# Optimization experiments

Measured on AMD Instinct MI355X. Metric: run time of the kernel, lower is better.

## Reference

```python
import jax, jax.numpy as jnp
import numpy as np

N_HEADS = 32
KV_HEADS = 8
HEAD_DIM = 128
N_REP = N_HEADS // KV_HEADS


def _rope(x, cos, sin):
    # x: [b, s, h, d]; cos/sin: [s, d//2]
    xr = x[..., 0::2]
    xi = x[..., 1::2]
    c = cos[None, :, None, :]
    s = sin[None, :, None, :]
    or_ = xr * c - xi * s
    oi_ = xr * s + xi * c
    return jnp.stack([or_, oi_], axis=-1).reshape(x.shape)


def setup_inputs() -> dict:
    key = jax.random.key(0)
    ks = jax.random.split(key, 9)
    b, s, dim = 32, 1, 4096
    scale = 1.0 / np.sqrt(dim)
    inp = {
        "x": jax.random.normal(ks[0], (b, s, dim), jnp.float32),
        "wq": jax.random.normal(ks[1], (4096, 4096), jnp.float32) * scale,
        "wk": jax.random.normal(ks[2], (1024, 4096), jnp.float32) * scale,
        "wv": jax.random.normal(ks[3], (1024, 4096), jnp.float32) * scale,
        "wo": jax.random.normal(ks[4], (4096, 4096), jnp.float32) * scale,
        "freqs_cos": jax.random.uniform(ks[5], (s, HEAD_DIM // 2), jnp.float32),
        "freqs_sin": jax.random.uniform(ks[6], (s, HEAD_DIM // 2), jnp.float32),
        "cache_k": jax.random.normal(ks[7], (32, 2048, KV_HEADS, HEAD_DIM), jnp.float32),
        "cache_v": jax.random.normal(ks[8], (32, 2048, KV_HEADS, HEAD_DIM), jnp.float32),
        "start_pos": 2047,
    }
    return inp


def reference(x, wq, wk, wv, wo, freqs_cos, freqs_sin, cache_k, cache_v, start_pos):
    b, s, dim = x.shape
    # projections (nn.Linear: y = x @ W^T)
    xq = (x @ wq.T).reshape(b, s, N_HEADS, HEAD_DIM)
    xk = (x @ wk.T).reshape(b, s, KV_HEADS, HEAD_DIM)
    xv = (x @ wv.T).reshape(b, s, KV_HEADS, HEAD_DIM)
    # inline RoPE on q and k
    xq = _rope(xq, freqs_cos, freqs_sin)
    xk = _rope(xk, freqs_cos, freqs_sin)
    # KV-cache write (start_pos is a static Python int)
    cache_k = cache_k.at[:b, start_pos:start_pos + s].set(xk)
    cache_v = cache_v.at[:b, start_pos:start_pos + s].set(xv)
    t = start_pos + s
    keys = cache_k[:b, :t]    # [b, t, kv, d]
    values = cache_v[:b, :t]  # [b, t, kv, d]
    # GQA: group queries per kv head instead of materializing repeat_kv copies
    q = xq.reshape(b, s, KV_HEADS, N_REP, HEAD_DIM)
    scores = jnp.einsum("bqhrd,bkhd->bhrqk", q, keys) / np.sqrt(HEAD_DIM)
    probs = jax.nn.softmax(scores.astype(jnp.float32), axis=-1).astype(xq.dtype)
    out = jnp.einsum("bhrqk,bkhd->bqhrd", probs, values)
    out = out.reshape(b, s, N_HEADS * HEAD_DIM)
    return out @ wo.T
```

## Files before the change

kernel.cpp:

```cpp
#include <hip/hip_runtime.h>
#include <hip/hip_bf16.h>
#include <math.h>

#define KSPLIT 16
#define KCHUNK 256
#define BJ 128

__global__ __launch_bounds__(256) void gemv_part_kernel(
    const float* __restrict__ x,
    const float* __restrict__ w0,
    const float* __restrict__ w1,
    const float* __restrict__ w2,
    int jb1, int jb2,
    int off0, int off1, int off2,
    int ncols,
    float* __restrict__ part)
{
  __shared__ float xt[KCHUNK][32];
  int jb = blockIdx.x, ks = blockIdx.y;
  int k0 = ks * KCHUNK;
  const float* w; int colOff, jbase;
  if (jb < jb1)      { w = w0; colOff = off0; jbase = jb * BJ; }
  else if (jb < jb2) { w = w1; colOff = off1; jbase = (jb - jb1) * BJ; }
  else               { w = w2; colOff = off2; jbase = (jb - jb2) * BJ; }
  int tid = threadIdx.x;
  {
    int b = tid & 31, kg = tid >> 5;
    const float* xr = x + (size_t)b * 4096 + k0 + kg * 32;
    #pragma unroll
    for (int i = 0; i < 8; i++) {
      float4 v = *(const float4*)(xr + i * 4);
      int k = kg * 32 + i * 4;
      xt[k + 0][b] = v.x; xt[k + 1][b] = v.y;
      xt[k + 2][b] = v.z; xt[k + 3][b] = v.w;
    }
  }
  __syncthreads();
  int bg = tid & 7, jg = tid >> 3;
  const float* wb = w + (size_t)(jbase + jg * 4) * 4096 + k0;
  float acc[4][4] = {};
  #pragma unroll 4
  for (int k4 = 0; k4 < KCHUNK / 4; k4++) {
    float wr[4][4], xv[4][4];
    #pragma unroll
    for (int jj = 0; jj < 4; jj++) {
      float4 t = *(const float4*)(wb + (size_t)jj * 4096 + k4 * 4);
      wr[jj][0] = t.x; wr[jj][1] = t.y; wr[jj][2] = t.z; wr[jj][3] = t.w;
    }
    #pragma unroll
    for (int c = 0; c < 4; c++) {
      float4 t = *(const float4*)(&xt[k4 * 4 + c][bg * 4]);
      xv[c][0] = t.x; xv[c][1] = t.y; xv[c][2] = t.z; xv[c][3] = t.w;
    }
    #pragma unroll
    for (int jj = 0; jj < 4; jj++)
      #pragma unroll
      for (int bb = 0; bb < 4; bb++)
        acc[jj][bb] += wr[jj][0] * xv[0][bb] + wr[jj][1] * xv[1][bb]
                     + wr[jj][2] * xv[2][bb] + wr[jj][3] * xv[3][bb];
  }
  #pragma unroll
  for (int jj = 0; jj < 4; jj++) {
    int col = colOff + jbase + jg * 4 + jj;
    #pragma unroll
    for (int bb = 0; bb < 4; bb++) {
      int b_ = bg * 4 + bb;
      part[((size_t)ks * 32 + b_) * ncols + col] = acc[jj][bb];
    }
  }
}

__global__ __launch_bounds__(256) void reduce_rope_kernel(
    const float* __restrict__ part, int ncols,
    const float* __restrict__ cosv, const float* __restrict__ sinv,
    int ropeEnd, float* __restrict__ outb)
{
  int idx = blockIdx.x * 256 + threadIdx.x;
  int np = ncols >> 1;
  int b = idx / np;
  int cp = idx - b * np;
  int col = cp * 2;
  float e = 0.f, o = 0.f;
  #pragma unroll
  for (int ks = 0; ks < KSPLIT; ks++) {
    float2 v = *(const float2*)(part + ((size_t)ks * 32 + b) * ncols + col);
    e += v.x; o += v.y;
  }
  if (col < ropeEnd) {
    int fi = (col & 127) >> 1;
    float c = cosv[fi], s = sinv[fi];
    float ne = e * c - o * s;
    float no = e * s + o * c;
    e = ne; o = no;
  }
  *(float2*)(outb + (size_t)b * ncols + col) = make_float2(e, o);
}

__global__ __launch_bounds__(256) void attn_kernel(
    const float* __restrict__ qkv,
    const float* __restrict__ cache_k,
    const float* __restrict__ cache_v,
    const int* __restrict__ spp,
    float* __restrict__ attn_part)
{
  __shared__ float q_s[4][128];
  __shared__ float kn_s[128], vn_s[128];
  __shared__ float p_s[4][4][64];
  __shared__ float comb_m[4][4], comb_l[4][4];
  __shared__ float comb_o[4][4][128];
  int bid = blockIdx.x;
  int ts = bid & 1, h = (bid >> 1) & 7, b = bid >> 4;
  int sp = *spp;
  const float scale = 0.088388347648318447f;
  int tid = threadIdx.x;
  {
    int i0 = tid * 2;
    int r = i0 >> 7, d = i0 & 127;
    q_s[r][d]     = qkv[(size_t)b * 6144 + (h * 4 + r) * 128 + d]     * scale;
    q_s[r][d + 1] = qkv[(size_t)b * 6144 + (h * 4 + r) * 128 + d + 1] * scale;
  }
  if (tid < 128) {
    kn_s[tid] = qkv[(size_t)b * 6144 + 4096 + h * 128 + tid];
    vn_s[tid] = qkv[(size_t)b * 6144 + 5120 + h * 128 + tid];
  }
  __syncthreads();
  int wave = tid >> 6, lane = tid & 63;
  int base0 = ts * 1024 + wave * 256;
  float m[4]    = {-INFINITY, -INFINITY, -INFINITY, -INFINITY};
  float lsum[4] = {0.f, 0.f, 0.f, 0.f};
  float o0[4] = {0.f, 0.f, 0.f, 0.f}, o1[4] = {0.f, 0.f, 0.f, 0.f};
  const float* Kb = cache_k + (size_t)b * 2048 * 1024 + h * 128;
  const float* Vb = cache_v + (size_t)b * 2048 * 1024 + h * 128;

  for (int c = 0; c < 4; c++) {
    int tbase = base0 + c * 64;
    int t = tbase + lane;
    float s[4];
    if (t < sp) {
      s[0] = s[1] = s[2] = s[3] = 0.f;
      const float* Kr = Kb + (size_t)t * 1024;
      #pragma unroll 8
      for (int d4 = 0; d4 < 32; d4++) {
        float4 kv = *(const float4*)(Kr + d4 * 4);
        #pragma unroll
        for (int r = 0; r < 4; r++) {
          float4 qv = *(const float4*)(&q_s[r][d4 * 4]);
          s[r] += kv.x * qv.x + kv.y * qv.y + kv.z * qv.z + kv.w * qv.w;
        }
      }
    } else {
      s[0] = s[1] = s[2] = s[3] = -INFINITY;
    }
    #pragma unroll
    for (int r = 0; r < 4; r++) {
      float cm = s[r];
      #pragma unroll
      for (int off = 32; off >= 1; off >>= 1) cm = fmaxf(cm, __shfl_xor(cm, off));
      float nm = fmaxf(m[r], cm);
      float alpha, p;
      if (nm == -INFINITY) { alpha = 1.f; p = 0.f; }
      else {
        alpha = __expf(m[r] - nm);
        p = (s[r] == -INFINITY) ? 0.f : __expf(s[r] - nm);
      }
      m[r] = nm;
      lsum[r] = lsum[r] * alpha + p;
      o0[r] *= alpha; o1[r] *= alpha;
      p_s[wave][r][lane] = p;
    }
    #pragma unroll 8
    for (int tt = 0; tt < 64; tt++) {
      const float* Vr = Vb + (size_t)(tbase + tt) * 1024;
      float2 vv = *(const float2*)(Vr + lane * 2);
      #pragma unroll
      for (int r = 0; r < 4; r++) {
        float p = p_s[wave][r][tt];
        o0[r] += p * vv.x; o1[r] += p * vv.y;
      }
    }
  }

  if (wave == 0 && sp >= ts * 1024 && sp < ts * 1024 + 1024) {
    float sNew[4];
    #pragma unroll
    for (int r = 0; r < 4; r++) {
      float a = q_s[r][lane * 2] * kn_s[lane * 2]
              + q_s[r][lane * 2 + 1] * kn_s[lane * 2 + 1];
      #pragma unroll
      for (int off = 32; off >= 1; off >>= 1) a += __shfl_xor(a, off);
      sNew[r] = a;
    }
    #pragma unroll
    for (int r = 0; r < 4; r++) {
      float nm = fmaxf(m[r], sNew[r]);
      float alpha = (m[r] == -INFINITY) ? 0.f : __expf(m[r] - nm);
      float p = __expf(sNew[r] - nm);
      m[r] = nm;
      lsum[r] = lsum[r] * alpha + ((lane == 0) ? p : 0.f);
      o0[r] = o0[r] * alpha + p * vn_s[lane * 2];
      o1[r] = o1[r] * alpha + p * vn_s[lane * 2 + 1];
    }
  }

  #pragma unroll
  for (int r = 0; r < 4; r++) {
    float L = lsum[r];
    #pragma unroll
    for (int off = 32; off >= 1; off >>= 1) L += __shfl_xor(L, off);
    if (lane == 0) { comb_m[wave][r] = m[r]; comb_l[wave][r] = L; }
    comb_o[wave][r][lane * 2]     = o0[r];
    comb_o[wave][r][lane * 2 + 1] = o1[r];
  }
  __syncthreads();
  {
    int r = tid >> 6, dp = tid & 63;
    float gm = fmaxf(fmaxf(comb_m[0][r], comb_m[1][r]),
                     fmaxf(comb_m[2][r], comb_m[3][r]));
    float L = 0.f, O0 = 0.f, O1 = 0.f;
    #pragma unroll
    for (int wv = 0; wv < 4; wv++) {
      float mm = comb_m[wv][r];
      float al = (mm == -INFINITY) ? 0.f : __expf(mm - gm);
      L  += comb_l[wv][r] * al;
      O0 += comb_o[wv][r][dp * 2]     * al;
      O1 += comb_o[wv][r][dp * 2 + 1] * al;
    }
    float* ap = attn_part + ((((size_t)ts * 32 + b) * 8 + h) * 4 + r) * 130;
    if (dp == 0) { ap[0] = gm; ap[1] = L; }
    ap[2 + dp * 2] = O0;
    ap[3 + dp * 2] = O1;
  }
}

__global__ __launch_bounds__(256) void attn_combine_kernel(
    const float* __restrict__ attn_part, float* __restrict__ attn)
{
  int idx = blockIdx.x * 256 + threadIdx.x;
  int d = idx & 127;
  int r = (idx >> 7) & 3;
  int h = (idx >> 9) & 7;
  int b = idx >> 12;
  const float* p0 = attn_part + (((size_t)(0 * 32 + b) * 8 + h) * 4 + r) * 130;
  const float* p1 = attn_part + (((size_t)(1 * 32 + b) * 8 + h) * 4 + r) * 130;
  float m0 = p0[0], l0 = p0[1], m1 = p1[0], l1 = p1[1];
  float gm = fmaxf(m0, m1);
  float a0 = __expf(m0 - gm), a1 = __expf(m1 - gm);
  float L = l0 * a0 + l1 * a1;
  float o = p0[2 + d] * a0 + p1[2 + d] * a1;
  attn[idx] = o / L;
}

extern "C" void kernel_launch(void* const* d_in, const int* in_sizes, int n_in,
                              void* d_out, int out_size, void* d_ws, size_t ws_size,
                              hipStream_t stream)
{
  const float* x   = (const float*)d_in[0];
  const float* wq  = (const float*)d_in[1];
  const float* wk  = (const float*)d_in[2];
  const float* wv  = (const float*)d_in[3];
  const float* wo  = (const float*)d_in[4];
  const float* fc  = (const float*)d_in[5];
  const float* fs  = (const float*)d_in[6];
  const float* ck  = (const float*)d_in[7];
  const float* cv  = (const float*)d_in[8];
  const int*   spp = (const int*)d_in[9];
  float* out = (float*)d_out;

  float* ws = (float*)d_ws;
  float* qkv_part  = ws;
  float* out_part  = ws;
  float* qkvbuf    = ws + 3145728;
  float* attn_part = qkvbuf + 196608;
  float* attnbuf   = attn_part + 266240;

  gemv_part_kernel<<<dim3(48, KSPLIT), 256, 0, stream>>>(
      x, wq, wk, wv, 32, 40, 0, 4096, 5120, 6144, qkv_part);
  reduce_rope_kernel<<<384, 256, 0, stream>>>(qkv_part, 6144, fc, fs, 5120, qkvbuf);
  attn_kernel<<<512, 256, 0, stream>>>(qkvbuf, ck, cv, spp, attn_part);
  attn_combine_kernel<<<512, 256, 0, stream>>>(attn_part, attnbuf);
  gemv_part_kernel<<<dim3(32, KSPLIT), 256, 0, stream>>>(
      attnbuf, wo, wo, wo, 32, 32, 0, 0, 0, 4096, out_part);
  reduce_rope_kernel<<<256, 256, 0, stream>>>(out_part, 4096, fc, fs, 0, out);
}
```

Before: 204.5 us.

## Split attention over four KV segments and widen V loads to float4

The attention kernel now splits the 2048-token KV range into four segments instead of two, doubling the block count to 1024, and the combine kernel merges four partial softmax states. The V accumulation loop has each half-wave take alternating tokens and read float4 instead of float2, then merges the halves with a cross-lane shuffle. Launch bounds request 4 blocks per CU. The aim is more parallelism and wider memory transactions for the bandwidth-bound KV read, at the cost of more partial-state traffic and extra shuffles.

```diff
diff --git a/kernel.cpp b/kernel.cpp
--- a/kernel.cpp
+++ b/kernel.cpp
@@ -5,6 +5,7 @@
 #define KSPLIT 16
 #define KCHUNK 256
 #define BJ 128
+#define TSPLIT 4
 
 __global__ __launch_bounds__(256) void gemv_part_kernel(
     const float* __restrict__ x,
@@ -96,7 +97,7 @@
   *(float2*)(outb + (size_t)b * ncols + col) = make_float2(e, o);
 }
 
-__global__ __launch_bounds__(256) void attn_kernel(
+__global__ __launch_bounds__(256, 4) void attn_kernel(
     const float* __restrict__ qkv,
     const float* __restrict__ cache_k,
     const float* __restrict__ cache_v,
@@ -109,7 +110,7 @@
   __shared__ float comb_m[4][4], comb_l[4][4];
   __shared__ float comb_o[4][4][128];
   int bid = blockIdx.x;
-  int ts = bid & 1, h = (bid >> 1) & 7, b = bid >> 4;
+  int ts = bid & (TSPLIT - 1), h = (bid >> 2) & 7, b = bid >> 5;
   int sp = *spp;
   const float scale = 0.088388347648318447f;
   int tid = threadIdx.x;
@@ -125,14 +126,15 @@
   }
   __syncthreads();
   int wave = tid >> 6, lane = tid & 63;
-  int base0 = ts * 1024 + wave * 256;
+  int half = lane >> 5, dq = lane & 31;
+  int base0 = ts * 512 + wave * 128;
   float m[4]    = {-INFINITY, -INFINITY, -INFINITY, -INFINITY};
   float lsum[4] = {0.f, 0.f, 0.f, 0.f};
-  float o0[4] = {0.f, 0.f, 0.f, 0.f}, o1[4] = {0.f, 0.f, 0.f, 0.f};
+  float o[4][4] = {};
   const float* Kb = cache_k + (size_t)b * 2048 * 1024 + h * 128;
   const float* Vb = cache_v + (size_t)b * 2048 * 1024 + h * 128;
 
-  for (int c = 0; c < 4; c++) {
+  for (int c = 0; c < 2; c++) {
     int tbase = base0 + c * 64;
     int t = tbase + lane;
     float s[4];
@@ -165,22 +167,24 @@
       }
       m[r] = nm;
       lsum[r] = lsum[r] * alpha + p;
-      o0[r] *= alpha; o1[r] *= alpha;
+      #pragma unroll
+      for (int j = 0; j < 4; j++) o[r][j] *= alpha;
       p_s[wave][r][lane] = p;
     }
     #pragma unroll 8
-    for (int tt = 0; tt < 64; tt++) {
-      const float* Vr = Vb + (size_t)(tbase + tt) * 1024;
-      float2 vv = *(const float2*)(Vr + lane * 2);
+    for (int tt = 0; tt < 32; tt++) {
+      int tcur = tbase + tt * 2 + half;
+      float4 vv = *(const float4*)(Vb + (size_t)tcur * 1024 + dq * 4);
       #pragma unroll
       for (int r = 0; r < 4; r++) {
-        float p = p_s[wave][r][tt];
-        o0[r] += p * vv.x; o1[r] += p * vv.y;
+        float p = p_s[wave][r][tt * 2 + half];
+        o[r][0] += p * vv.x; o[r][1] += p * vv.y;
+        o[r][2] += p * vv.z; o[r][3] += p * vv.w;
       }
     }
   }
 
-  if (wave == 0 && sp >= ts * 1024 && sp < ts * 1024 + 1024) {
+  if (wave == 0 && sp >= ts * 512 && sp < ts * 512 + 512) {
     float sNew[4];
     #pragma unroll
     for (int r = 0; r < 4; r++) {
@@ -197,8 +201,10 @@
       float p = __expf(sNew[r] - nm);
       m[r] = nm;
       lsum[r] = lsum[r] * alpha + ((lane == 0) ? p : 0.f);
-      o0[r] = o0[r] * alpha + p * vn_s[lane * 2];
-      o1[r] = o1[r] * alpha + p * vn_s[lane * 2 + 1];
+      float sel = (half == 0) ? p : 0.f;
+      #pragma unroll
+      for (int j = 0; j < 4; j++)
+        o[r][j] = o[r][j] * alpha + sel * vn_s[dq * 4 + j];
     }
   }
 
@@ -207,9 +213,13 @@
     float L = lsum[r];
     #pragma unroll
     for (int off = 32; off >= 1; off >>= 1) L += __shfl_xor(L, off);
+    #pragma unroll
+    for (int j = 0; j < 4; j++) o[r][j] += __shfl_xor(o[r][j], 32);
     if (lane == 0) { comb_m[wave][r] = m[r]; comb_l[wave][r] = L; }
-    comb_o[wave][r][lane * 2]     = o0[r];
-    comb_o[wave][r][lane * 2 + 1] = o1[r];
+    if (half == 0) {
+      #pragma unroll
+      for (int j = 0; j < 4; j++) comb_o[wave][r][dq * 4 + j] = o[r][j];
+    }
   }
   __syncthreads();
   {
@@ -240,14 +250,22 @@
   int r = (idx >> 7) & 3;
   int h = (idx >> 9) & 7;
   int b = idx >> 12;
-  const float* p0 = attn_part + (((size_t)(0 * 32 + b) * 8 + h) * 4 + r) * 130;
-  const float* p1 = attn_part + (((size_t)(1 * 32 + b) * 8 + h) * 4 + r) * 130;
-  float m0 = p0[0], l0 = p0[1], m1 = p1[0], l1 = p1[1];
-  float gm = fmaxf(m0, m1);
-  float a0 = __expf(m0 - gm), a1 = __expf(m1 - gm);
-  float L = l0 * a0 + l1 * a1;
-  float o = p0[2 + d] * a0 + p1[2 + d] * a1;
-  attn[idx] = o / L;
+  float mv[TSPLIT], lv[TSPLIT], ov[TSPLIT];
+  float gm = -INFINITY;
+  #pragma unroll
+  for (int ts = 0; ts < TSPLIT; ts++) {
+    const float* ap = attn_part + (((size_t)(ts * 32 + b) * 8 + h) * 4 + r) * 130;
+    mv[ts] = ap[0]; lv[ts] = ap[1]; ov[ts] = ap[2 + d];
+    gm = fmaxf(gm, mv[ts]);
+  }
+  float L = 0.f, O = 0.f;
+  #pragma unroll
+  for (int ts = 0; ts < TSPLIT; ts++) {
+    float al = (mv[ts] == -INFINITY) ? 0.f : __expf(mv[ts] - gm);
+    L += lv[ts] * al;
+    O += ov[ts] * al;
+  }
+  attn[idx] = O / L;
 }
 
 extern "C" void kernel_launch(void* const* d_in, const int* in_sizes, int n_in,
@@ -271,12 +289,12 @@
   float* out_part  = ws;
   float* qkvbuf    = ws + 3145728;
   float* attn_part = qkvbuf + 196608;
-  float* attnbuf   = attn_part + 266240;
+  float* attnbuf   = attn_part + 532480;
 
   gemv_part_kernel<<<dim3(48, KSPLIT), 256, 0, stream>>>(
       x, wq, wk, wv, 32, 40, 0, 4096, 5120, 6144, qkv_part);
   reduce_rope_kernel<<<384, 256, 0, stream>>>(qkv_part, 6144, fc, fs, 5120, qkvbuf);
-  attn_kernel<<<512, 256, 0, stream>>>(qkvbuf, ck, cv, spp, attn_part);
+  attn_kernel<<<1024, 256, 0, stream>>>(qkvbuf, ck, cv, spp, attn_part);
   attn_combine_kernel<<<512, 256, 0, stream>>>(attn_part, attnbuf);
   gemv_part_kernel<<<dim3(32, KSPLIT), 256, 0, stream>>>(
       attnbuf, wo, wo, wo, 32, 32, 0, 0, 0, 4096, out_part);
```

Measured after the change: 211.4 us. 1.03x slower.
